# Kernel tuning notes

Measured on AMD Instinct MI355X. Metric: run time of the kernel, lower is better.

Reference implementation:

```python
import jax, jax.numpy as jnp
import numpy as np

DIM = 128
HEADS = 4
WS = (8, 7, 7)  # window_size (d, h, w)
B = 256         # batch * num_windows
N = WS[0] * WS[1] * WS[2]  # 392 tokens per window


def _relative_position_index(ws):
    # Faithful replication of get_coords_grid + index math (including its
    # axis-order quirks): meshgrid over (w, h, d) with indexing='ij'.
    d, h, w = ws
    gw, gh, gd = np.meshgrid(np.arange(w), np.arange(h), np.arange(d), indexing='ij')
    coords = np.stack([gw, gh, gd], axis=0).reshape(3, -1)          # (3, N)
    rel = coords[:, :, None] - coords[:, None, :]                    # (3, N, N)
    rel = rel.transpose(1, 2, 0).copy()                              # (N, N, 3)
    rel[:, :, 0] += ws[0] - 1
    rel[:, :, 1] += ws[1] - 1
    rel[:, :, 2] += ws[2] - 1
    rl = (2 * d - 1, 2 * h - 1, 2 * w - 1)
    idx = rel[:, :, 0] * rl[1] * rl[2] + rel[:, :, 1] * rl[2] + rel[:, :, 2]
    return idx.reshape(-1).astype(np.int32), int(np.prod(rl))


def setup_inputs() -> dict:
    key = jax.random.key(0)
    k0, k1, k2, k3, k4, k5 = jax.random.split(key, 6)
    idx, table_size = _relative_position_index(WS)
    s = 1.0 / np.sqrt(DIM)
    return {
        "hidden_states": jax.random.normal(k0, (B, WS[0], WS[1], WS[2], DIM), jnp.float32),
        "W_qkv_w": jax.random.normal(k1, (3 * DIM, DIM), jnp.float32) * s,
        "W_qkv_b": jax.random.normal(k2, (3 * DIM,), jnp.float32) * s,
        "proj_w": jax.random.normal(k3, (DIM, DIM), jnp.float32) * s,
        "proj_b": jax.random.normal(k4, (DIM,), jnp.float32) * s,
        "rpb_table": jax.random.normal(k5, (HEADS, table_size), jnp.float32),
        "rel_index": jnp.asarray(idx),
    }


def reference(hidden_states, W_qkv_w, W_qkv_b, proj_w, proj_b, rpb_table, rel_index):
    b, nz, ny, nx, dim = hidden_states.shape
    H = HEADS
    dh = dim // H
    n = nz * ny * nx
    # QKV projection, split into q/k/v of shape (b, H, n, dh)
    qkv = hidden_states @ W_qkv_w.T + W_qkv_b            # (b, nz, ny, nx, 3*dim)
    qkv = qkv.reshape(b, n, 3, H, dh).transpose(2, 0, 3, 1, 4)
    q, k, v = qkv[0], qkv[1], qkv[2]
    scores = jnp.einsum('bhnd,bhmd->bhnm', q, k) / (dh ** 0.5)
    # Bias: gather (H, n*n) then raw row-major reshape to (1, n, n, H),
    # then permute to (1, H, n, n) -- exactly as the torch code does.
    bias = rpb_table[:, rel_index].reshape(1, n, n, H).transpose(0, 3, 1, 2)
    probs = jax.nn.softmax(scores + bias, axis=-1)
    ctx = jnp.einsum('bhnm,bhmd->bhnd', probs, v)        # (b, H, n, dh)
    ctx = ctx.transpose(0, 2, 1, 3).reshape(b, nz, ny, nx, dim)
    return ctx @ proj_w.T + proj_b
```

## Files before the change

kernel.cpp:

```cpp
#include <hip/hip_runtime.h>
#include <hip/hip_bf16.h>


typedef __attribute__((ext_vector_type(8))) short bf16x8;
typedef __attribute__((ext_vector_type(4))) float f32x4;
typedef __attribute__((ext_vector_type(4))) short s16x4;
typedef __attribute__((ext_vector_type(2))) unsigned int u32x2;

#define NTOK 392
#define NN (NTOK * NTOK)
#define TABLE 2535
#define SCALE 0.17677669529663689f

__device__ __forceinline__ unsigned short f2bf(float f) {
  union { float f; unsigned u; } v; v.f = f;
  unsigned r = v.u + 0x7FFFu + ((v.u >> 16) & 1u);
  return (unsigned short)(r >> 16);
}
__device__ __forceinline__ unsigned short f2bf_rn(float f) {
  union { __hip_bfloat16 h; unsigned short u; } v;
  v.h = __float2bfloat16(f);
  return v.u;
}
__device__ __forceinline__ float b2f(short s) {
  union { unsigned u; float f; } v;
  v.u = ((unsigned)(unsigned short)s) << 16;
  return v.f;
}
__device__ __forceinline__ unsigned pk2(float lo, float hi) {
  return (unsigned)f2bf_rn(lo) | ((unsigned)f2bf_rn(hi) << 16);
}

__global__ __launch_bounds__(256) void wcvt_kernel(
    const float* __restrict__ Wqkv, const float* __restrict__ Wp,
    unsigned short* __restrict__ wqbf, unsigned short* __restrict__ wpbf) {
  int g = blockIdx.x * 256 + threadIdx.x;
  const float* src; unsigned short* dst; int off;
  if (g < 12288) { src = Wqkv; dst = wqbf; off = g * 4; }
  else           { src = Wp;   dst = wpbf; off = (g - 12288) * 4; }
  f32x4 v = *(const f32x4*)(src + off);
  s16x4 o;
  o[0] = (short)f2bf(v[0]); o[1] = (short)f2bf(v[1]);
  o[2] = (short)f2bf(v[2]); o[3] = (short)f2bf(v[3]);
  *(s16x4*)(dst + off) = o;
}

__global__ __launch_bounds__(256) void biaspre_kernel(
    const float* __restrict__ rpb, const int* __restrict__ relidx,
    unsigned short* __restrict__ biaspre) {
  int g = blockIdx.x * 256 + threadIdx.x;
  if (g >= 640000) return;
  int r = g & 3, lane = (g >> 2) & 63;
  int t = g >> 8;
  int jt = t % 25; int t2 = t / 25;
  int rb = t2 % 25; int h = t2 / 25;
  int q = rb * 16 + (lane & 15); if (q > 391) q = 391;
  int k = jt * 16 + (lane >> 4) * 4 + r; if (k > 391) k = 391;
  int f = q * (NTOK * 4) + k * 4 + h;
  int hs = f / NN; int p = f - hs * NN;
  biaspre[g] = f2bf(rpb[hs * TABLE + relidx[p]]);
}

__global__ __launch_bounds__(256, 4) void qkv_gemm(
    const float* __restrict__ hidden, const unsigned short* __restrict__ wqbf,
    const float* __restrict__ bqkv,
    unsigned short* __restrict__ qbuf, unsigned short* __restrict__ kbuf,
    unsigned short* __restrict__ vtbuf) {
  __shared__ unsigned short Abf[128][34];
  __shared__ unsigned short Bbf[128][34];
  __shared__ unsigned short Epi[128][132];
  const int tid = threadIdx.x;
  const int w = tid >> 6, lane = tid & 63, l15 = lane & 15, lhi = lane >> 4;
  const int mblk = blockIdx.x, s = blockIdx.y;
  const int wm = w >> 1, wn = w & 1;

  f32x4 acc[4][4];
#pragma unroll
  for (int m = 0; m < 4; ++m)
#pragma unroll
    for (int n = 0; n < 4; ++n) acc[m][n] = 0.0f;

  for (int kk = 0; kk < 4; ++kk) {
#pragma unroll
    for (int it = 0; it < 4; ++it) {
      int i = it * 256 + tid;
      int row = i >> 3, c4 = i & 7;
      f32x4 v = *(const f32x4*)(
          hidden + ((size_t)(mblk * 128 + row)) * 128 + kk * 32 + c4 * 4);
      u32x2 p; p[0] = pk2(v[0], v[1]); p[1] = pk2(v[2], v[3]);
      *(u32x2*)&Abf[row][c4 * 4] = p;
    }
#pragma unroll
    for (int it = 0; it < 2; ++it) {
      int i = it * 256 + tid;
      int row = i >> 2, c = i & 3;
      *(bf16x8*)&Bbf[row][c * 8] = *(const bf16x8*)(
          wqbf + ((size_t)(s * 128 + row)) * 128 + kk * 32 + c * 8);
    }
    __syncthreads();
    bf16x8 af[4], bf[4];
#pragma unroll
    for (int m = 0; m < 4; ++m) af[m] = *(const bf16x8*)&Abf[wm * 64 + m * 16 + l15][lhi * 8];
#pragma unroll
    for (int n = 0; n < 4; ++n) bf[n] = *(const bf16x8*)&Bbf[wn * 64 + n * 16 + l15][lhi * 8];
#pragma unroll
    for (int m = 0; m < 4; ++m)
#pragma unroll
      for (int n = 0; n < 4; ++n)
        acc[m][n] = __builtin_amdgcn_mfma_f32_16x16x32_bf16(af[m], bf[n], acc[m][n], 0, 0, 0);
    __syncthreads();
  }

  float bias_n[4];
#pragma unroll
  for (int n = 0; n < 4; ++n) bias_n[n] = bqkv[s * 128 + wn * 64 + n * 16 + l15];

  if (s < 2) {
    const float mul = (s == 0) ? SCALE : 1.0f;
#pragma unroll
    for (int m = 0; m < 4; ++m)
#pragma unroll
      for (int n = 0; n < 4; ++n)
#pragma unroll
        for (int r = 0; r < 4; ++r)
          Epi[wm * 64 + m * 16 + lhi * 4 + r][wn * 64 + n * 16 + l15] =
              f2bf_rn((acc[m][n][r] + bias_n[n]) * mul);
    __syncthreads();
    unsigned short* dst = (s == 0) ? qbuf : kbuf;
#pragma unroll
    for (int it = 0; it < 8; ++it) {
      int idx = it * 256 + tid;
      int row = idx >> 4, c = idx & 15;
      *(bf16x8*)&dst[((size_t)(mblk * 128 + row)) * 128 + c * 8] =
          *(const bf16x8*)&Epi[row][c * 8];
    }
  } else {
#pragma unroll
    for (int m = 0; m < 4; ++m)
#pragma unroll
      for (int n = 0; n < 4; ++n)
#pragma unroll
        for (int r = 0; r < 4; ++r)
          Epi[wn * 64 + n * 16 + l15][wm * 64 + m * 16 + lhi * 4 + r] =
              f2bf_rn(acc[m][n][r] + bias_n[n]);
    __syncthreads();
#pragma unroll
    for (int it = 0; it < 8; ++it) {
      int idx = it * 256 + tid;
      int fe = idx >> 4, ch = idx & 15;
      int tg = mblk * 128 + ch * 8;
      int wb = tg / 392;
      int n0 = tg - wb * 392;
      *(bf16x8*)&vtbuf[(((size_t)wb * 4 + (fe >> 5)) * 32 + (fe & 31)) * NTOK + n0] =
          *(const bf16x8*)&Epi[fe][ch * 8];
    }
  }
}

__global__ __launch_bounds__(256, 4) void attn_kernel(
    const unsigned short* __restrict__ qbuf, const unsigned short* __restrict__ kbuf,
    const unsigned short* __restrict__ vtbuf, const unsigned short* __restrict__ biaspre,
    unsigned short* __restrict__ ctxbuf) {
  __shared__ unsigned short Ksh[400][40];
  __shared__ unsigned int Psh[4][16][20];

  const int tid = threadIdx.x;
  const int w = tid >> 6, lane = tid & 63;
  const int l15 = lane & 15, lhi = lane >> 4;
  const int bh = blockIdx.x;
  const int h = bh & 3, b = bh >> 2;
  const size_t vtb = (size_t)bh * (NTOK * 32);

  for (int i = tid; i < 3136; i += 256) {
    int row = i >> 3, c4 = i & 7;
    *(s16x4*)&Ksh[row][c4 * 4] =
        *(const s16x4*)(kbuf + ((size_t)(b * NTOK + row)) * 128 + h * 32 + c4 * 4);
  }
  { int row = 392 + (tid >> 5); Ksh[row][tid & 31] = 0; }
  __syncthreads();

  const unsigned short* vbase = vtbuf + vtb;
  const s16x4* bias_lane =
      (const s16x4*)(biaspre + (size_t)h * 25 * 25 * 256 + (size_t)lane * 4);

  for (int rb = w; rb < 25; rb += 4) {
    int qrow = rb * 16 + l15; if (qrow > 391) qrow = 391;
    bf16x8 qf = *(const bf16x8*)(
        qbuf + ((size_t)(b * NTOK + qrow)) * 128 + h * 32 + lhi * 8);
    const s16x4* bp = bias_lane + (size_t)rb * 25 * 64;

    f32x4 o0 = 0.0f, o1 = 0.0f;
    float ssum = 0.f;

    for (int g = 0; g < 12; ++g) {
      int jt0 = 2 * g, jt1 = 2 * g + 1;
      bf16x8 kf0 = *(const bf16x8*)&Ksh[jt0 * 16 + l15][lhi * 8];
      bf16x8 kf1 = *(const bf16x8*)&Ksh[jt1 * 16 + l15][lhi * 8];
      f32x4 s0 = __builtin_amdgcn_mfma_f32_16x16x32_bf16(kf0, qf, (f32x4)0.f, 0, 0, 0);
      f32x4 s1 = __builtin_amdgcn_mfma_f32_16x16x32_bf16(kf1, qf, (f32x4)0.f, 0, 0, 0);
      s16x4 bv0 = bp[jt0 * 64];
      s16x4 bv1 = bp[jt1 * 64];
      float e00 = __expf(s0[0] + b2f(bv0[0])), e01 = __expf(s0[1] + b2f(bv0[1]));
      float e02 = __expf(s0[2] + b2f(bv0[2])), e03 = __expf(s0[3] + b2f(bv0[3]));
      float e10 = __expf(s1[0] + b2f(bv1[0])), e11 = __expf(s1[1] + b2f(bv1[1]));
      float e12 = __expf(s1[2] + b2f(bv1[2])), e13 = __expf(s1[3] + b2f(bv1[3]));
      ssum += (e00 + e01 + e02 + e03) + (e10 + e11 + e12 + e13);
      u32x2 wlo; wlo[0] = pk2(e00, e01); wlo[1] = pk2(e02, e03);
      u32x2 whi; whi[0] = pk2(e10, e11); whi[1] = pk2(e12, e13);
      *(u32x2*)&Psh[w][l15][lhi * 2] = wlo;
      *(u32x2*)&Psh[w][l15][8 + lhi * 2] = whi;
      bf16x8 pf = *(const bf16x8*)&Psh[w][l15][lhi * 4];
      bf16x8 vf0 = *(const bf16x8*)(vbase + (size_t)l15 * NTOK + g * 32 + lhi * 8);
      bf16x8 vf1 = *(const bf16x8*)(vbase + (size_t)(16 + l15) * NTOK + g * 32 + lhi * 8);
      o0 = __builtin_amdgcn_mfma_f32_16x16x32_bf16(pf, vf0, o0, 0, 0, 0);
      o1 = __builtin_amdgcn_mfma_f32_16x16x32_bf16(pf, vf1, o1, 0, 0, 0);
    }
    {
      bf16x8 kf0 = *(const bf16x8*)&Ksh[384 + l15][lhi * 8];
      f32x4 s0 = __builtin_amdgcn_mfma_f32_16x16x32_bf16(kf0, qf, (f32x4)0.f, 0, 0, 0);
      s16x4 bv0 = bp[24 * 64];
      float e00 = __expf(s0[0] + b2f(bv0[0])), e01 = __expf(s0[1] + b2f(bv0[1]));
      float e02 = __expf(s0[2] + b2f(bv0[2])), e03 = __expf(s0[3] + b2f(bv0[3]));
      if (lhi >= 2) { e00 = 0.f; e01 = 0.f; e02 = 0.f; e03 = 0.f; }
      ssum += (e00 + e01) + (e02 + e03);
      u32x2 wlo; wlo[0] = pk2(e00, e01); wlo[1] = pk2(e02, e03);
      u32x2 whi; whi[0] = 0u; whi[1] = 0u;
      *(u32x2*)&Psh[w][l15][lhi * 2] = wlo;
      *(u32x2*)&Psh[w][l15][8 + lhi * 2] = whi;
      bf16x8 pf = *(const bf16x8*)&Psh[w][l15][lhi * 4];
      bf16x8 vf0 = *(const bf16x8*)(vbase + (size_t)l15 * NTOK + 384 + lhi * 8);
      bf16x8 vf1 = *(const bf16x8*)(vbase + (size_t)(16 + l15) * NTOK + 384 + lhi * 8);
      o0 = __builtin_amdgcn_mfma_f32_16x16x32_bf16(pf, vf0, o0, 0, 0, 0);
      o1 = __builtin_amdgcn_mfma_f32_16x16x32_bf16(pf, vf1, o1, 0, 0, 0);
    }

    ssum += __shfl_xor(ssum, 16);
    ssum += __shfl_xor(ssum, 32);
    float rtot = 1.f / ssum;
    float rr[4];
#pragma unroll
    for (int r = 0; r < 4; ++r) rr[r] = __shfl(rtot, lhi * 4 + r);

#pragma unroll
    for (int r = 0; r < 4; ++r) {
      int row = rb * 16 + lhi * 4 + r;
      if (row < NTOK) {
        unsigned short* crow = ctxbuf + ((size_t)(b * NTOK) + row) * 128 + h * 32;
        crow[l15] = f2bf_rn(o0[r] * rr[r]);
        crow[16 + l15] = f2bf_rn(o1[r] * rr[r]);
      }
    }
  }
}

__global__ __launch_bounds__(256, 4) void proj_gemm(
    const unsigned short* __restrict__ ctxbuf, const unsigned short* __restrict__ wpbf,
    const float* __restrict__ bp, float* __restrict__ out) {
  __shared__ unsigned short Abf[128][34];
  __shared__ unsigned short Bbf[128][34];
  const int tid = threadIdx.x;
  const int w = tid >> 6, lane = tid & 63, l15 = lane & 15, lhi = lane >> 4;
  const int mblk = blockIdx.x;
  const int wm = w >> 1, wn = w & 1;

  f32x4 acc[4][4];
#pragma unroll
  for (int m = 0; m < 4; ++m)
#pragma unroll
    for (int n = 0; n < 4; ++n) acc[m][n] = 0.0f;

  for (int kk = 0; kk < 4; ++kk) {
#pragma unroll
    for (int it = 0; it < 2; ++it) {
      int i = it * 256 + tid;
      int row = i >> 2, c = i & 3;
      *(bf16x8*)&Abf[row][c * 8] = *(const bf16x8*)(
          ctxbuf + ((size_t)(mblk * 128 + row)) * 128 + kk * 32 + c * 8);
      *(bf16x8*)&Bbf[row][c * 8] = *(const bf16x8*)(
          wpbf + ((size_t)row) * 128 + kk * 32 + c * 8);
    }
    __syncthreads();
    bf16x8 af[4], bf[4];
#pragma unroll
    for (int m = 0; m < 4; ++m) af[m] = *(const bf16x8*)&Abf[wm * 64 + m * 16 + l15][lhi * 8];
#pragma unroll
    for (int n = 0; n < 4; ++n) bf[n] = *(const bf16x8*)&Bbf[wn * 64 + n * 16 + l15][lhi * 8];
#pragma unroll
    for (int m = 0; m < 4; ++m)
#pragma unroll
      for (int n = 0; n < 4; ++n)
        acc[m][n] = __builtin_amdgcn_mfma_f32_16x16x32_bf16(af[m], bf[n], acc[m][n], 0, 0, 0);
    __syncthreads();
  }

  float bias_n[4];
#pragma unroll
  for (int n = 0; n < 4; ++n) bias_n[n] = bp[wn * 64 + n * 16 + l15];
#pragma unroll
  for (int m = 0; m < 4; ++m)
#pragma unroll
    for (int n = 0; n < 4; ++n)
#pragma unroll
      for (int r = 0; r < 4; ++r) {
        int row = mblk * 128 + wm * 64 + m * 16 + lhi * 4 + r;
        __builtin_nontemporal_store(
            acc[m][n][r] + bias_n[n],
            &out[(size_t)row * 128 + wn * 64 + n * 16 + l15]);
      }
}

extern "C" void kernel_launch(void* const* d_in, const int* in_sizes, int n_in,
                              void* d_out, int out_size, void* d_ws, size_t ws_size,
                              hipStream_t stream) {
  const float* hidden = (const float*)d_in[0];
  const float* Wqkv = (const float*)d_in[1];
  const float* bqkv = (const float*)d_in[2];
  const float* Wp = (const float*)d_in[3];
  const float* bp = (const float*)d_in[4];
  const float* rpb = (const float*)d_in[5];
  const int* relidx = (const int*)d_in[6];

  unsigned short* qbuf = (unsigned short*)d_ws;
  unsigned short* kbuf = qbuf + 12845056;
  unsigned short* vtbuf = kbuf + 12845056;
  unsigned short* ctxbuf = vtbuf + 12845056 + 1024;
  unsigned short* biaspre = ctxbuf + 12845056;
  unsigned short* wqbf = biaspre + 640000;
  unsigned short* wpbf = wqbf + 49152;

  wcvt_kernel<<<64, 256, 0, stream>>>(Wqkv, Wp, wqbf, wpbf);
  biaspre_kernel<<<2500, 256, 0, stream>>>(rpb, relidx, biaspre);
  qkv_gemm<<<dim3(784, 3), 256, 0, stream>>>(hidden, wqbf, bqkv, qbuf, kbuf, vtbuf);
  attn_kernel<<<1024, 256, 0, stream>>>(qbuf, kbuf, vtbuf, biaspre, ctxbuf);
  proj_gemm<<<784, 256, 0, stream>>>(ctxbuf, wpbf, bp, (float*)d_out);
}
```

Before: 166.0 us.

## Process two query row-blocks per wave, fold bias into MFMA and use exp2

The attention loop now has each wave handle two 16-row query blocks together, so every K-fragment and V-fragment load is shared between them, with a separate tail path for row block 24. The relative-position bias is passed as the MFMA accumulator input instead of being added after the score. log2(e) is pre-multiplied into the Q scale and the bias table so the softmax can use exp2f. The aim is fewer K/V loads per FLOP, more independent MFMA work in flight, and fewer VALU ops. The cost is higher register pressure and doubled per-wave P scratch in LDS, plus a load imbalance because wave 0 alone handles the last row block.

```diff
diff --git a/kernel.cpp b/kernel.cpp
--- a/kernel.cpp
+++ b/kernel.cpp
@@ -11,6 +11,8 @@
 #define NN (NTOK * NTOK)
 #define TABLE 2535
 #define SCALE 0.17677669529663689f
+#define LOG2E 1.4426950408889634f
+#define QSCALE (0.17677669529663689f * 1.4426950408889634f)
 
 __device__ __forceinline__ unsigned short f2bf(float f) {
   union { float f; unsigned u; } v; v.f = f;
@@ -58,7 +60,7 @@
   int k = jt * 16 + (lane >> 4) * 4 + r; if (k > 391) k = 391;
   int f = q * (NTOK * 4) + k * 4 + h;
   int hs = f / NN; int p = f - hs * NN;
-  biaspre[g] = f2bf(rpb[hs * TABLE + relidx[p]]);
+  biaspre[g] = f2bf(rpb[hs * TABLE + relidx[p]] * LOG2E);
 }
 
 __global__ __launch_bounds__(256, 4) void qkv_gemm(
@@ -116,7 +118,7 @@
   for (int n = 0; n < 4; ++n) bias_n[n] = bqkv[s * 128 + wn * 64 + n * 16 + l15];
 
   if (s < 2) {
-    const float mul = (s == 0) ? SCALE : 1.0f;
+    const float mul = (s == 0) ? QSCALE : 1.0f;
 #pragma unroll
     for (int m = 0; m < 4; ++m)
 #pragma unroll
@@ -162,14 +164,13 @@
     const unsigned short* __restrict__ vtbuf, const unsigned short* __restrict__ biaspre,
     unsigned short* __restrict__ ctxbuf) {
   __shared__ unsigned short Ksh[400][40];
-  __shared__ unsigned int Psh[4][16][20];
+  __shared__ unsigned int Psh[8][16][20];
 
   const int tid = threadIdx.x;
   const int w = tid >> 6, lane = tid & 63;
   const int l15 = lane & 15, lhi = lane >> 4;
   const int bh = blockIdx.x;
   const int h = bh & 3, b = bh >> 2;
-  const size_t vtb = (size_t)bh * (NTOK * 32);
 
   for (int i = tid; i < 3136; i += 256) {
     int row = i >> 3, c4 = i & 7;
@@ -179,37 +180,156 @@
   { int row = 392 + (tid >> 5); Ksh[row][tid & 31] = 0; }
   __syncthreads();
 
-  const unsigned short* vbase = vtbuf + vtb;
+  const unsigned short* vbase = vtbuf + (size_t)bh * (NTOK * 32);
   const s16x4* bias_lane =
       (const s16x4*)(biaspre + (size_t)h * 25 * 25 * 256 + (size_t)lane * 4);
-
-  for (int rb = w; rb < 25; rb += 4) {
+  unsigned int* PA = &Psh[2 * w][0][0];
+  unsigned int* PB = &Psh[2 * w + 1][0][0];
+
+  for (int t = 0; t < 3; ++t) {
+    const int rbA = w + t * 8, rbB = w + 4 + t * 8;
+    bf16x8 qfA = *(const bf16x8*)(
+        qbuf + ((size_t)(b * NTOK + rbA * 16 + l15)) * 128 + h * 32 + lhi * 8);
+    bf16x8 qfB = *(const bf16x8*)(
+        qbuf + ((size_t)(b * NTOK + rbB * 16 + l15)) * 128 + h * 32 + lhi * 8);
+    const s16x4* bpA = bias_lane + (size_t)rbA * 25 * 64;
+    const s16x4* bpB = bias_lane + (size_t)rbB * 25 * 64;
+
+    f32x4 o0A = 0.0f, o1A = 0.0f, o0B = 0.0f, o1B = 0.0f;
+    float ssA = 0.f, ssB = 0.f;
+
+    for (int g = 0; g < 12; ++g) {
+      int jt0 = 2 * g, jt1 = 2 * g + 1;
+      bf16x8 kf0 = *(const bf16x8*)&Ksh[jt0 * 16 + l15][lhi * 8];
+      bf16x8 kf1 = *(const bf16x8*)&Ksh[jt1 * 16 + l15][lhi * 8];
+      bf16x8 vf0 = *(const bf16x8*)(vbase + (size_t)l15 * NTOK + g * 32 + lhi * 8);
+      bf16x8 vf1 = *(const bf16x8*)(vbase + (size_t)(16 + l15) * NTOK + g * 32 + lhi * 8);
+      s16x4 bA0 = bpA[jt0 * 64], bA1 = bpA[jt1 * 64];
+      s16x4 bB0 = bpB[jt0 * 64], bB1 = bpB[jt1 * 64];
+      f32x4 cA0, cA1, cB0, cB1;
+#pragma unroll
+      for (int r = 0; r < 4; ++r) {
+        cA0[r] = b2f(bA0[r]); cA1[r] = b2f(bA1[r]);
+        cB0[r] = b2f(bB0[r]); cB1[r] = b2f(bB1[r]);
+      }
+      f32x4 sA0 = __builtin_amdgcn_mfma_f32_16x16x32_bf16(kf0, qfA, cA0, 0, 0, 0);
+      f32x4 sA1 = __builtin_amdgcn_mfma_f32_16x16x32_bf16(kf1, qfA, cA1, 0, 0, 0);
+      f32x4 sB0 = __builtin_amdgcn_mfma_f32_16x16x32_bf16(kf0, qfB, cB0, 0, 0, 0);
+      f32x4 sB1 = __builtin_amdgcn_mfma_f32_16x16x32_bf16(kf1, qfB, cB1, 0, 0, 0);
+
+      float eA00 = exp2f(sA0[0]), eA01 = exp2f(sA0[1]);
+      float eA02 = exp2f(sA0[2]), eA03 = exp2f(sA0[3]);
+      float eA10 = exp2f(sA1[0]), eA11 = exp2f(sA1[1]);
+      float eA12 = exp2f(sA1[2]), eA13 = exp2f(sA1[3]);
+      float eB00 = exp2f(sB0[0]), eB01 = exp2f(sB0[1]);
+      float eB02 = exp2f(sB0[2]), eB03 = exp2f(sB0[3]);
+      float eB10 = exp2f(sB1[0]), eB11 = exp2f(sB1[1]);
+      float eB12 = exp2f(sB1[2]), eB13 = exp2f(sB1[3]);
+      ssA += (eA00 + eA01 + eA02 + eA03) + (eA10 + eA11 + eA12 + eA13);
+      ssB += (eB00 + eB01 + eB02 + eB03) + (eB10 + eB11 + eB12 + eB13);
+
+      u32x2 wloA; wloA[0] = pk2(eA00, eA01); wloA[1] = pk2(eA02, eA03);
+      u32x2 whiA; whiA[0] = pk2(eA10, eA11); whiA[1] = pk2(eA12, eA13);
+      u32x2 wloB; wloB[0] = pk2(eB00, eB01); wloB[1] = pk2(eB02, eB03);
+      u32x2 whiB; whiB[0] = pk2(eB10, eB11); whiB[1] = pk2(eB12, eB13);
+      *(u32x2*)&PA[l15 * 20 + lhi * 2] = wloA;
+      *(u32x2*)&PA[l15 * 20 + 8 + lhi * 2] = whiA;
+      *(u32x2*)&PB[l15 * 20 + lhi * 2] = wloB;
+      *(u32x2*)&PB[l15 * 20 + 8 + lhi * 2] = whiB;
+      bf16x8 pfA = *(const bf16x8*)&PA[l15 * 20 + lhi * 4];
+      bf16x8 pfB = *(const bf16x8*)&PB[l15 * 20 + lhi * 4];
+      o0A = __builtin_amdgcn_mfma_f32_16x16x32_bf16(pfA, vf0, o0A, 0, 0, 0);
+      o1A = __builtin_amdgcn_mfma_f32_16x16x32_bf16(pfA, vf1, o1A, 0, 0, 0);
+      o0B = __builtin_amdgcn_mfma_f32_16x16x32_bf16(pfB, vf0, o0B, 0, 0, 0);
+      o1B = __builtin_amdgcn_mfma_f32_16x16x32_bf16(pfB, vf1, o1B, 0, 0, 0);
+    }
+    {
+      bf16x8 kf0 = *(const bf16x8*)&Ksh[384 + l15][lhi * 8];
+      s16x4 bA0 = bpA[24 * 64], bB0 = bpB[24 * 64];
+      f32x4 cA0, cB0;
+#pragma unroll
+      for (int r = 0; r < 4; ++r) { cA0[r] = b2f(bA0[r]); cB0[r] = b2f(bB0[r]); }
+      f32x4 sA0 = __builtin_amdgcn_mfma_f32_16x16x32_bf16(kf0, qfA, cA0, 0, 0, 0);
+      f32x4 sB0 = __builtin_amdgcn_mfma_f32_16x16x32_bf16(kf0, qfB, cB0, 0, 0, 0);
+      float eA0 = exp2f(sA0[0]), eA1 = exp2f(sA0[1]);
+      float eA2 = exp2f(sA0[2]), eA3 = exp2f(sA0[3]);
+      float eB0 = exp2f(sB0[0]), eB1 = exp2f(sB0[1]);
+      float eB2 = exp2f(sB0[2]), eB3 = exp2f(sB0[3]);
+      if (lhi >= 2) {
+        eA0 = 0.f; eA1 = 0.f; eA2 = 0.f; eA3 = 0.f;
+        eB0 = 0.f; eB1 = 0.f; eB2 = 0.f; eB3 = 0.f;
+      }
+      ssA += (eA0 + eA1) + (eA2 + eA3);
+      ssB += (eB0 + eB1) + (eB2 + eB3);
+      u32x2 wloA; wloA[0] = pk2(eA0, eA1); wloA[1] = pk2(eA2, eA3);
+      u32x2 wloB; wloB[0] = pk2(eB0, eB1); wloB[1] = pk2(eB2, eB3);
+      u32x2 z; z[0] = 0u; z[1] = 0u;
+      *(u32x2*)&PA[l15 * 20 + lhi * 2] = wloA;
+      *(u32x2*)&PA[l15 * 20 + 8 + lhi * 2] = z;
+      *(u32x2*)&PB[l15 * 20 + lhi * 2] = wloB;
+      *(u32x2*)&PB[l15 * 20 + 8 + lhi * 2] = z;
+      bf16x8 pfA = *(const bf16x8*)&PA[l15 * 20 + lhi * 4];
+      bf16x8 pfB = *(const bf16x8*)&PB[l15 * 20 + lhi * 4];
+      bf16x8 vf0 = *(const bf16x8*)(vbase + (size_t)l15 * NTOK + 384 + lhi * 8);
+      bf16x8 vf1 = *(const bf16x8*)(vbase + (size_t)(16 + l15) * NTOK + 384 + lhi * 8);
+      o0A = __builtin_amdgcn_mfma_f32_16x16x32_bf16(pfA, vf0, o0A, 0, 0, 0);
+      o1A = __builtin_amdgcn_mfma_f32_16x16x32_bf16(pfA, vf1, o1A, 0, 0, 0);
+      o0B = __builtin_amdgcn_mfma_f32_16x16x32_bf16(pfB, vf0, o0B, 0, 0, 0);
+      o1B = __builtin_amdgcn_mfma_f32_16x16x32_bf16(pfB, vf1, o1B, 0, 0, 0);
+    }
+
+#pragma unroll
+    for (int i = 0; i < 2; ++i) {
+      float ss = (i == 0) ? ssA : ssB;
+      f32x4 o0 = (i == 0) ? o0A : o0B;
+      f32x4 o1 = (i == 0) ? o1A : o1B;
+      int rb = (i == 0) ? rbA : rbB;
+      ss += __shfl_xor(ss, 16);
+      ss += __shfl_xor(ss, 32);
+      float rtot = 1.f / ss;
+      float rr[4];
+#pragma unroll
+      for (int r = 0; r < 4; ++r) rr[r] = __shfl(rtot, lhi * 4 + r);
+#pragma unroll
+      for (int r = 0; r < 4; ++r) {
+        int row = rb * 16 + lhi * 4 + r;
+        unsigned short* crow = ctxbuf + ((size_t)(b * NTOK) + row) * 128 + h * 32;
+        crow[l15] = f2bf_rn(o0[r] * rr[r]);
+        crow[16 + l15] = f2bf_rn(o1[r] * rr[r]);
+      }
+    }
+  }
+
+  if (w == 0) {
+    const int rb = 24;
     int qrow = rb * 16 + l15; if (qrow > 391) qrow = 391;
     bf16x8 qf = *(const bf16x8*)(
         qbuf + ((size_t)(b * NTOK + qrow)) * 128 + h * 32 + lhi * 8);
     const s16x4* bp = bias_lane + (size_t)rb * 25 * 64;
 
     f32x4 o0 = 0.0f, o1 = 0.0f;
-    float ssum = 0.f;
+    float ss = 0.f;
 
     for (int g = 0; g < 12; ++g) {
       int jt0 = 2 * g, jt1 = 2 * g + 1;
       bf16x8 kf0 = *(const bf16x8*)&Ksh[jt0 * 16 + l15][lhi * 8];
       bf16x8 kf1 = *(const bf16x8*)&Ksh[jt1 * 16 + l15][lhi * 8];
-      f32x4 s0 = __builtin_amdgcn_mfma_f32_16x16x32_bf16(kf0, qf, (f32x4)0.f, 0, 0, 0);
-      f32x4 s1 = __builtin_amdgcn_mfma_f32_16x16x32_bf16(kf1, qf, (f32x4)0.f, 0, 0, 0);
-      s16x4 bv0 = bp[jt0 * 64];
-      s16x4 bv1 = bp[jt1 * 64];
-      float e00 = __expf(s0[0] + b2f(bv0[0])), e01 = __expf(s0[1] + b2f(bv0[1]));
-      float e02 = __expf(s0[2] + b2f(bv0[2])), e03 = __expf(s0[3] + b2f(bv0[3]));
-      float e10 = __expf(s1[0] + b2f(bv1[0])), e11 = __expf(s1[1] + b2f(bv1[1]));
-      float e12 = __expf(s1[2] + b2f(bv1[2])), e13 = __expf(s1[3] + b2f(bv1[3]));
-      ssum += (e00 + e01 + e02 + e03) + (e10 + e11 + e12 + e13);
+      s16x4 bv0 = bp[jt0 * 64], bv1 = bp[jt1 * 64];
+      f32x4 c0, c1;
+#pragma unroll
+      for (int r = 0; r < 4; ++r) { c0[r] = b2f(bv0[r]); c1[r] = b2f(bv1[r]); }
+      f32x4 s0 = __builtin_amdgcn_mfma_f32_16x16x32_bf16(kf0, qf, c0, 0, 0, 0);
+      f32x4 s1 = __builtin_amdgcn_mfma_f32_16x16x32_bf16(kf1, qf, c1, 0, 0, 0);
+      float e00 = exp2f(s0[0]), e01 = exp2f(s0[1]);
+      float e02 = exp2f(s0[2]), e03 = exp2f(s0[3]);
+      float e10 = exp2f(s1[0]), e11 = exp2f(s1[1]);
+      float e12 = exp2f(s1[2]), e13 = exp2f(s1[3]);
+      ss += (e00 + e01 + e02 + e03) + (e10 + e11 + e12 + e13);
       u32x2 wlo; wlo[0] = pk2(e00, e01); wlo[1] = pk2(e02, e03);
       u32x2 whi; whi[0] = pk2(e10, e11); whi[1] = pk2(e12, e13);
-      *(u32x2*)&Psh[w][l15][lhi * 2] = wlo;
-      *(u32x2*)&Psh[w][l15][8 + lhi * 2] = whi;
-      bf16x8 pf = *(const bf16x8*)&Psh[w][l15][lhi * 4];
+      *(u32x2*)&PA[l15 * 20 + lhi * 2] = wlo;
+      *(u32x2*)&PA[l15 * 20 + 8 + lhi * 2] = whi;
+      bf16x8 pf = *(const bf16x8*)&PA[l15 * 20 + lhi * 4];
       bf16x8 vf0 = *(const bf16x8*)(vbase + (size_t)l15 * NTOK + g * 32 + lhi * 8);
       bf16x8 vf1 = *(const bf16x8*)(vbase + (size_t)(16 + l15) * NTOK + g * 32 + lhi * 8);
       o0 = __builtin_amdgcn_mfma_f32_16x16x32_bf16(pf, vf0, o0, 0, 0, 0);
@@ -217,30 +337,32 @@
     }
     {
       bf16x8 kf0 = *(const bf16x8*)&Ksh[384 + l15][lhi * 8];
-      f32x4 s0 = __builtin_amdgcn_mfma_f32_16x16x32_bf16(kf0, qf, (f32x4)0.f, 0, 0, 0);
       s16x4 bv0 = bp[24 * 64];
-      float e00 = __expf(s0[0] + b2f(bv0[0])), e01 = __expf(s0[1] + b2f(bv0[1]));
-      float e02 = __expf(s0[2] + b2f(bv0[2])), e03 = __expf(s0[3] + b2f(bv0[3]));
+      f32x4 c0;
+#pragma unroll
+      for (int r = 0; r < 4; ++r) c0[r] = b2f(bv0[r]);
+      f32x4 s0 = __builtin_amdgcn_mfma_f32_16x16x32_bf16(kf0, qf, c0, 0, 0, 0);
+      float e00 = exp2f(s0[0]), e01 = exp2f(s0[1]);
+      float e02 = exp2f(s0[2]), e03 = exp2f(s0[3]);
       if (lhi >= 2) { e00 = 0.f; e01 = 0.f; e02 = 0.f; e03 = 0.f; }
-      ssum += (e00 + e01) + (e02 + e03);
+      ss += (e00 + e01) + (e02 + e03);
       u32x2 wlo; wlo[0] = pk2(e00, e01); wlo[1] = pk2(e02, e03);
-      u32x2 whi; whi[0] = 0u; whi[1] = 0u;
-      *(u32x2*)&Psh[w][l15][lhi * 2] = wlo;
-      *(u32x2*)&Psh[w][l15][8 + lhi * 2] = whi;
-      bf16x8 pf = *(const bf16x8*)&Psh[w][l15][lhi * 4];
+      u32x2 z; z[0] = 0u; z[1] = 0u;
+      *(u32x2*)&PA[l15 * 20 + lhi * 2] = wlo;
+      *(u32x2*)&PA[l15 * 20 + 8 + lhi * 2] = z;
+      bf16x8 pf = *(const bf16x8*)&PA[l15 * 20 + lhi * 4];
       bf16x8 vf0 = *(const bf16x8*)(vbase + (size_t)l15 * NTOK + 384 + lhi * 8);
       bf16x8 vf1 = *(const bf16x8*)(vbase + (size_t)(16 + l15) * NTOK + 384 + lhi * 8);
       o0 = __builtin_amdgcn_mfma_f32_16x16x32_bf16(pf, vf0, o0, 0, 0, 0);
       o1 = __builtin_amdgcn_mfma_f32_16x16x32_bf16(pf, vf1, o1, 0, 0, 0);
     }
 
-    ssum += __shfl_xor(ssum, 16);
-    ssum += __shfl_xor(ssum, 32);
-    float rtot = 1.f / ssum;
+    ss += __shfl_xor(ss, 16);
+    ss += __shfl_xor(ss, 32);
+    float rtot = 1.f / ss;
     float rr[4];
 #pragma unroll
     for (int r = 0; r < 4; ++r) rr[r] = __shfl(rtot, lhi * 4 + r);
-
 #pragma unroll
     for (int r = 0; r < 4; ++r) {
       int row = rb * 16 + lhi * 4 + r;
```

After: 185.9 us. +12.0%, slower.
